# Kernel tuning notes

Hardware: AMD Instinct MI355X
Metric: run time of the kernel (lower is better)

Reference implementation:

```python
import jax, jax.numpy as jnp
import numpy as np

EMBED_DIM = 1024
NUM_HEADS = 16
HEAD_DIM = EMBED_DIM // NUM_HEADS


def setup_inputs() -> dict:
    key = jax.random.key(0)
    k1, k2, k3, k4, k5 = jax.random.split(key, 5)
    B, N, D = 2, 2048, EMBED_DIM
    s = 1.0 / np.sqrt(D)
    x = jax.random.normal(k1, (B, N, D), dtype=jnp.float32)
    qkv_w = jax.random.uniform(k2, (3 * D, D), minval=-s, maxval=s, dtype=jnp.float32)
    qkv_b = jax.random.uniform(k3, (3 * D,), minval=-s, maxval=s, dtype=jnp.float32)
    proj_w = jax.random.uniform(k4, (D, D), minval=-s, maxval=s, dtype=jnp.float32)
    proj_b = jax.random.uniform(k5, (D,), minval=-s, maxval=s, dtype=jnp.float32)
    return {"x": x, "qkv_w": qkv_w, "qkv_b": qkv_b, "proj_w": proj_w, "proj_b": proj_b}


def reference(x, qkv_w, qkv_b, proj_w, proj_b):
    B, N, D = x.shape
    H, Hd = NUM_HEADS, HEAD_DIM
    scale = Hd ** (-0.5)
    # QKV projection (torch Linear: x @ W.T + b)
    qkv = x @ qkv_w.T + qkv_b                      # [B, N, 3D]
    q, k, v = jnp.split(qkv, 3, axis=-1)
    def split_heads(t):
        return t.reshape(B, N, H, Hd).transpose(0, 2, 1, 3)  # [B, H, N, Hd]
    q, k, v = map(split_heads, (q, k, v))
    attn = jnp.einsum("bhqd,bhkd->bhqk", q, k) * scale       # [B, H, N, N]
    attn = jax.nn.softmax(attn, axis=-1)
    out = jnp.einsum("bhqk,bhkd->bhqd", attn, v)             # [B, H, N, Hd]
    out = out.transpose(0, 2, 1, 3).reshape(B, N, D)
    return out @ proj_w.T + proj_b
```

## Files before the change

kernel.cpp:

```cpp
#include <hip/hip_runtime.h>
#include <hip/hip_bf16.h>


#define DEV __device__ __forceinline__

typedef __attribute__((ext_vector_type(8))) __bf16 bf16x8;
typedef __attribute__((ext_vector_type(4))) float f32x4;

static DEV unsigned short f2bf(float f) {
  unsigned u = __builtin_bit_cast(unsigned, f);
  u += 0x7FFFu + ((u >> 16) & 1u);
  return (unsigned short)(u >> 16);
}

static DEV void gld16(const void* g, void* l) {
  __builtin_amdgcn_global_load_lds(
      (const __attribute__((address_space(1))) unsigned int*)g,
      (__attribute__((address_space(3))) unsigned int*)l, 16, 0, 0);
}

static DEV f32x4 mfma16(bf16x8 a, bf16x8 b, f32x4 c) {
  return __builtin_amdgcn_mfma_f32_16x16x32_bf16(a, b, c, 0, 0, 0);
}

__global__ void k_f2bf(const float* __restrict__ s, unsigned short* __restrict__ d) {
  int i = (blockIdx.x * 256 + threadIdx.x) * 4;
  float4 v = *reinterpret_cast<const float4*>(s + i);
  union { unsigned short h[4]; uint2 u; } cv;
  cv.h[0] = f2bf(v.x); cv.h[1] = f2bf(v.y); cv.h[2] = f2bf(v.z); cv.h[3] = f2bf(v.w);
  *reinterpret_cast<uint2*>(d + i) = cv.u;
}

__global__ __launch_bounds__(256) void k_qkv(
    const unsigned short* __restrict__ A, const unsigned short* __restrict__ W,
    const float* __restrict__ bias, unsigned short* __restrict__ Qb,
    unsigned short* __restrict__ Kb, unsigned short* __restrict__ Vt) {
  const int K = 1024;
  __shared__ __align__(16) unsigned short As[128 * 32], Bs[128 * 32];
  const int tid = threadIdx.x, lane = tid & 63, wid = tid >> 6;
  const int wm = wid >> 1, wn = wid & 1, fr = lane & 15, fg = lane >> 4;
  const size_t bm = blockIdx.x, bn = blockIdx.y;
  const unsigned short* gA = A + bm * 128 * K;
  const unsigned short* gW = W + bn * 128 * K;
  f32x4 acc[4][4] = {};
  for (int k0 = 0; k0 < K; k0 += 32) {
#pragma unroll
    for (int c = 0; c < 2; ++c) {
      int bi = c * 4096 + wid * 1024 + lane * 16;
      int row = bi >> 6, ce = (bi & 63) >> 1;
      gld16(gA + (size_t)row * K + k0 + ce, As + c * 2048 + wid * 512);
      gld16(gW + (size_t)row * K + k0 + ce, Bs + c * 2048 + wid * 512);
    }
    __syncthreads();
    bf16x8 af[4], bw[4];
#pragma unroll
    for (int m = 0; m < 4; ++m)
      af[m] = *reinterpret_cast<const bf16x8*>(As + (wm * 64 + m * 16 + fr) * 32 + fg * 8);
#pragma unroll
    for (int n = 0; n < 4; ++n)
      bw[n] = *reinterpret_cast<const bf16x8*>(Bs + (wn * 64 + n * 16 + fr) * 32 + fg * 8);
#pragma unroll
    for (int m = 0; m < 4; ++m)
#pragma unroll
      for (int n = 0; n < 4; ++n)
        acc[m][n] = mfma16(af[m], bw[n], acc[m][n]);
    __syncthreads();
  }
  float bv[4];
#pragma unroll
  for (int n = 0; n < 4; ++n) bv[n] = bias[bn * 128 + wn * 64 + n * 16 + fr];
#pragma unroll
  for (int m = 0; m < 4; ++m)
#pragma unroll
    for (int n = 0; n < 4; ++n)
#pragma unroll
      for (int r = 0; r < 4; ++r) {
        int row = wm * 64 + m * 16 + fg * 4 + r;
        int token = (int)bm * 128 + row;
        int b_ = token >> 11, nn = token & 2047;
        int f = (int)bn * 128 + wn * 64 + n * 16 + fr;
        float val = acc[m][n][r] + bv[n];
        int t = f >> 10, d = f & 1023, h = d >> 6, hd = d & 63;
        size_t bh = (size_t)(b_ * 16 + h);
        if (t == 0)      Qb[(bh * 2048 + nn) * 64 + hd] = f2bf(val * 0.125f);
        else if (t == 1) Kb[(bh * 2048 + nn) * 64 + hd] = f2bf(val);
        else             Vt[(bh * 64 + hd) * 2048 + nn] = f2bf(val);
      }
}

__global__ __launch_bounds__(256) void k_attn(
    const unsigned short* __restrict__ Qb, const unsigned short* __restrict__ Kb,
    const unsigned short* __restrict__ Vt, unsigned short* __restrict__ Ob) {
  __shared__ __align__(16) unsigned short Ks[2][64 * 64];
  __shared__ __align__(16) unsigned short Vs[2][64 * 64];
  __shared__ __align__(16) unsigned short p_lds[4][16 * 64];
  const int tid = threadIdx.x, lane = tid & 63, w = tid >> 6;
  const int fr = lane & 15, fg = lane >> 4;
  const int bid = (int)(blockIdx.x & 7) * 128 + (int)(blockIdx.x >> 3);
  const int qt = bid & 31, bh = bid >> 5;
  const unsigned short* Qp = Qb + ((size_t)bh * 2048 + qt * 64 + w * 16) * 64;
  const unsigned short* Kp = Kb + (size_t)bh * 2048 * 64;
  const unsigned short* Vp = Vt + (size_t)bh * 64 * 2048;

  const int crow0 = w * 16 + (lane >> 3);
  bf16x8 qf[2];
#pragma unroll
  for (int ks = 0; ks < 2; ++ks)
    qf[ks] = *reinterpret_cast<const bf16x8*>(Qp + fr * 64 + ks * 32 + fg * 8);

  f32x4 accO[4] = {};
  float mrow = -1e30f, lpart = 0.f;

#define STAGE(bufi, kti)                                                      \
  {                                                                           \
    const unsigned short* Kt_ = Kp + (kti) * 64 * 64;                         \
    _Pragma("unroll")                                                         \
    for (int j = 0; j < 2; ++j) {                                             \
      int cr = crow0 + j * 8;                                                 \
      int cs = (lane & 7) ^ (cr & 7);                                         \
      gld16(Kt_ + cr * 64 + cs * 8, &Ks[bufi][(w * 2 + j) * 512]);            \
      gld16(Vp + (size_t)cr * 2048 + (kti) * 64 + cs * 8,                     \
            &Vs[bufi][(w * 2 + j) * 512]);                                    \
    }                                                                         \
  }

  STAGE(0, 0);
  __syncthreads();
  int buf = 0;
  for (int kt = 0; kt < 32; ++kt) {
    if (kt < 31) STAGE(buf ^ 1, kt + 1);
    f32x4 s[4] = {};
#pragma unroll
    for (int nf = 0; nf < 4; ++nf)
#pragma unroll
      for (int ks = 0; ks < 2; ++ks) {
        bf16x8 kf = *reinterpret_cast<const bf16x8*>(
            &Ks[buf][(nf * 16 + fr) * 64 + (((ks * 4 + fg) ^ (fr & 7)) * 8)]);
        s[nf] = mfma16(kf, qf[ks], s[nf]);
      }
    bf16x8 vf[2][4];
#pragma unroll
    for (int ks = 0; ks < 2; ++ks)
#pragma unroll
      for (int df = 0; df < 4; ++df)
        vf[ks][df] = *reinterpret_cast<const bf16x8*>(
            &Vs[buf][(df * 16 + fr) * 64 + (((ks * 4 + fg) ^ (fr & 7)) * 8)]);
    float mymax = fmaxf(
        fmaxf(fmaxf(fmaxf(s[0][0], s[0][1]), fmaxf(s[0][2], s[0][3])),
              fmaxf(fmaxf(s[1][0], s[1][1]), fmaxf(s[1][2], s[1][3]))),
        fmaxf(fmaxf(fmaxf(s[2][0], s[2][1]), fmaxf(s[2][2], s[2][3])),
              fmaxf(fmaxf(s[3][0], s[3][1]), fmaxf(s[3][2], s[3][3]))));
    if (!__all(mymax <= mrow + 8.0f)) {
      float pmax = mymax;
      pmax = fmaxf(pmax, __shfl_xor(pmax, 16));
      pmax = fmaxf(pmax, __shfl_xor(pmax, 32));
      float mnew = fmaxf(mrow, pmax);
      float sc = __expf(mrow - mnew);
      mrow = mnew;
      lpart *= sc;
      float scq[4];
#pragma unroll
      for (int r = 0; r < 4; ++r) scq[r] = __shfl(sc, fg * 4 + r);
#pragma unroll
      for (int df = 0; df < 4; ++df)
#pragma unroll
        for (int r = 0; r < 4; ++r) accO[df][r] *= scq[r];
    }
    float rs = 0.f;
#pragma unroll
    for (int nf = 0; nf < 4; ++nf)
#pragma unroll
      for (int r = 0; r < 4; ++r) {
        float p = __expf(s[nf][r] - mrow);
        s[nf][r] = p;
        rs += p;
      }
    lpart += rs;
#pragma unroll
    for (int nf = 0; nf < 4; ++nf) {
      union { unsigned short h[4]; uint2 u; } pk;
#pragma unroll
      for (int r = 0; r < 4; ++r) pk.h[r] = f2bf(s[nf][r]);
      *reinterpret_cast<uint2*>(
          &p_lds[w][fr * 64 + (((2 * nf + (fg >> 1)) ^ (fr & 7)) * 8) +
                   (fg & 1) * 4]) = pk.u;
    }
    bf16x8 pf[2];
#pragma unroll
    for (int ks = 0; ks < 2; ++ks)
      pf[ks] = *reinterpret_cast<const bf16x8*>(
          &p_lds[w][fr * 64 + (((ks * 4 + fg) ^ (fr & 7)) * 8)]);
#pragma unroll
    for (int df = 0; df < 4; ++df)
#pragma unroll
      for (int ks = 0; ks < 2; ++ks)
        accO[df] = mfma16(pf[ks], vf[ks][df], accO[df]);
    __syncthreads();
    buf ^= 1;
  }
#undef STAGE
  float lrow = lpart;
  lrow += __shfl_xor(lrow, 16);
  lrow += __shfl_xor(lrow, 32);
  float linv = 1.f / lrow;
  float lq[4];
#pragma unroll
  for (int r = 0; r < 4; ++r) lq[r] = __shfl(linv, fg * 4 + r);
  const int b_ = bh >> 4, h = bh & 15;
#pragma unroll
  for (int df = 0; df < 4; ++df)
#pragma unroll
    for (int r = 0; r < 4; ++r) {
      int nn = qt * 64 + w * 16 + fg * 4 + r;
      int d = df * 16 + fr;
      Ob[(size_t)(b_ * 2048 + nn) * 1024 + h * 64 + d] = f2bf(accO[df][r] * lq[r]);
    }
}

__global__ __launch_bounds__(256) void k_proj(
    const unsigned short* __restrict__ A, const unsigned short* __restrict__ W,
    const float* __restrict__ bias, float* __restrict__ out) {
  const int K = 1024;
  __shared__ __align__(16) unsigned short As[128 * 32], Bs[128 * 32];
  const int tid = threadIdx.x, lane = tid & 63, wid = tid >> 6;
  const int wm = wid >> 1, wn = wid & 1, fr = lane & 15, fg = lane >> 4;
  const size_t bm = blockIdx.x, bn = blockIdx.y;
  const unsigned short* gA = A + bm * 128 * K;
  const unsigned short* gW = W + bn * 128 * K;
  f32x4 acc[4][4] = {};
  for (int k0 = 0; k0 < K; k0 += 32) {
#pragma unroll
    for (int c = 0; c < 2; ++c) {
      int bi = c * 4096 + wid * 1024 + lane * 16;
      int row = bi >> 6, ce = (bi & 63) >> 1;
      gld16(gA + (size_t)row * K + k0 + ce, As + c * 2048 + wid * 512);
      gld16(gW + (size_t)row * K + k0 + ce, Bs + c * 2048 + wid * 512);
    }
    __syncthreads();
    bf16x8 af[4], bw[4];
#pragma unroll
    for (int m = 0; m < 4; ++m)
      af[m] = *reinterpret_cast<const bf16x8*>(As + (wm * 64 + m * 16 + fr) * 32 + fg * 8);
#pragma unroll
    for (int n = 0; n < 4; ++n)
      bw[n] = *reinterpret_cast<const bf16x8*>(Bs + (wn * 64 + n * 16 + fr) * 32 + fg * 8);
#pragma unroll
    for (int m = 0; m < 4; ++m)
#pragma unroll
      for (int n = 0; n < 4; ++n)
        acc[m][n] = mfma16(af[m], bw[n], acc[m][n]);
    __syncthreads();
  }
  float bv[4];
#pragma unroll
  for (int n = 0; n < 4; ++n) bv[n] = bias[bn * 128 + wn * 64 + n * 16 + fr];
#pragma unroll
  for (int m = 0; m < 4; ++m)
#pragma unroll
    for (int n = 0; n < 4; ++n)
#pragma unroll
      for (int r = 0; r < 4; ++r) {
        size_t token = bm * 128 + wm * 64 + m * 16 + fg * 4 + r;
        int f = (int)bn * 128 + wn * 64 + n * 16 + fr;
        out[token * 1024 + f] = acc[m][n][r] + bv[n];
      }
}

extern "C" void kernel_launch(void* const* d_in, const int* in_sizes, int n_in,
                              void* d_out, int out_size, void* d_ws, size_t ws_size,
                              hipStream_t stream) {
  const float* x      = (const float*)d_in[0];
  const float* qkv_w  = (const float*)d_in[1];
  const float* qkv_b  = (const float*)d_in[2];
  const float* proj_w = (const float*)d_in[3];
  const float* proj_b = (const float*)d_in[4];
  float* out = (float*)d_out;
  char* ws = (char*)d_ws;
  unsigned short* xb  = (unsigned short*)(ws);
  unsigned short* wqb = (unsigned short*)(ws + (size_t)(8u << 20));
  unsigned short* pwb = (unsigned short*)(ws + (size_t)(14u << 20));
  unsigned short* Qb  = (unsigned short*)(ws + (size_t)(16u << 20));
  unsigned short* Kb  = (unsigned short*)(ws + (size_t)(24u << 20));
  unsigned short* Vt  = (unsigned short*)(ws + (size_t)(32u << 20));
  unsigned short* Ob  = (unsigned short*)(ws + (size_t)(40u << 20));

  k_f2bf<<<4096, 256, 0, stream>>>(x, xb);
  k_f2bf<<<3072, 256, 0, stream>>>(qkv_w, wqb);
  k_f2bf<<<1024, 256, 0, stream>>>(proj_w, pwb);
  k_qkv<<<dim3(32, 24), 256, 0, stream>>>(xb, wqb, qkv_b, Qb, Kb, Vt);
  k_attn<<<1024, 256, 0, stream>>>(Qb, Kb, Vt, Ob);
  k_proj<<<dim3(32, 8), 256, 0, stream>>>(Ob, pwb, proj_b, out);
}
```

Measured before the change: 224.0 us.

## Fuse conversion kernels, use exp2 softmax, restructure attention double-buffer loop

```diff
diff --git a/kernel.cpp b/kernel.cpp
--- a/kernel.cpp
+++ b/kernel.cpp
@@ -13,6 +13,18 @@
   return (unsigned short)(u >> 16);
 }
 
+static DEV float fexp2(float x) {
+#if __has_builtin(__builtin_amdgcn_exp2f)
+  return __builtin_amdgcn_exp2f(x);
+#else
+  return __expf(x * 0.69314718055994531f);
+#endif
+}
+
+static DEV float max3(float a, float b, float c) {
+  return fmaxf(fmaxf(a, b), c);
+}
+
 static DEV void gld16(const void* g, void* l) {
   __builtin_amdgcn_global_load_lds(
       (const __attribute__((address_space(1))) unsigned int*)g,
@@ -23,8 +35,17 @@
   return __builtin_amdgcn_mfma_f32_16x16x32_bf16(a, b, c, 0, 0, 0);
 }
 
-__global__ void k_f2bf(const float* __restrict__ s, unsigned short* __restrict__ d) {
-  int i = (blockIdx.x * 256 + threadIdx.x) * 4;
+__global__ void k_conv(const float* __restrict__ x, const float* __restrict__ qw,
+                       const float* __restrict__ pw, unsigned short* __restrict__ xb,
+                       unsigned short* __restrict__ wqb, unsigned short* __restrict__ pwb) {
+  int b = blockIdx.x;
+  const float* s;
+  unsigned short* d;
+  int base;
+  if (b < 4096)      { s = x;  d = xb;  base = b; }
+  else if (b < 7168) { s = qw; d = wqb; base = b - 4096; }
+  else               { s = pw; d = pwb; base = b - 7168; }
+  int i = (base * 256 + threadIdx.x) * 4;
   float4 v = *reinterpret_cast<const float4*>(s + i);
   union { unsigned short h[4]; uint2 u; } cv;
   cv.h[0] = f2bf(v.x); cv.h[1] = f2bf(v.y); cv.h[2] = f2bf(v.z); cv.h[3] = f2bf(v.w);
@@ -66,33 +87,109 @@
         acc[m][n] = mfma16(af[m], bw[n], acc[m][n]);
     __syncthreads();
   }
+  const float QSCALE = 0.18033688011112043f;
   float bv[4];
 #pragma unroll
   for (int n = 0; n < 4; ++n) bv[n] = bias[bn * 128 + wn * 64 + n * 16 + fr];
 #pragma unroll
   for (int m = 0; m < 4; ++m)
 #pragma unroll
-    for (int n = 0; n < 4; ++n)
-#pragma unroll
-      for (int r = 0; r < 4; ++r) {
-        int row = wm * 64 + m * 16 + fg * 4 + r;
-        int token = (int)bm * 128 + row;
-        int b_ = token >> 11, nn = token & 2047;
-        int f = (int)bn * 128 + wn * 64 + n * 16 + fr;
-        float val = acc[m][n][r] + bv[n];
-        int t = f >> 10, d = f & 1023, h = d >> 6, hd = d & 63;
-        size_t bh = (size_t)(b_ * 16 + h);
-        if (t == 0)      Qb[(bh * 2048 + nn) * 64 + hd] = f2bf(val * 0.125f);
-        else if (t == 1) Kb[(bh * 2048 + nn) * 64 + hd] = f2bf(val);
-        else             Vt[(bh * 64 + hd) * 2048 + nn] = f2bf(val);
+    for (int n = 0; n < 4; ++n) {
+      int f = (int)bn * 128 + wn * 64 + n * 16 + fr;
+      int t = f >> 10, d = f & 1023, h = d >> 6, hd = d & 63;
+      int token0 = (int)bm * 128 + wm * 64 + m * 16 + fg * 4;
+      int b_ = token0 >> 11, nn0 = token0 & 2047;
+      size_t bh = (size_t)(b_ * 16 + h);
+      float v0 = acc[m][n][0] + bv[n], v1 = acc[m][n][1] + bv[n];
+      float v2 = acc[m][n][2] + bv[n], v3 = acc[m][n][3] + bv[n];
+      if (t == 0) {
+        unsigned short* q = Qb + (bh * 2048 + nn0) * 64 + hd;
+        q[0] = f2bf(v0 * QSCALE); q[64] = f2bf(v1 * QSCALE);
+        q[128] = f2bf(v2 * QSCALE); q[192] = f2bf(v3 * QSCALE);
+      } else if (t == 1) {
+        unsigned short* k = Kb + (bh * 2048 + nn0) * 64 + hd;
+        k[0] = f2bf(v0); k[64] = f2bf(v1); k[128] = f2bf(v2); k[192] = f2bf(v3);
+      } else {
+        union { unsigned short h[4]; uint2 u; } pk;
+        pk.h[0] = f2bf(v0); pk.h[1] = f2bf(v1);
+        pk.h[2] = f2bf(v2); pk.h[3] = f2bf(v3);
+        *reinterpret_cast<uint2*>(Vt + (bh * 64 + hd) * 2048 + nn0) = pk.u;
       }
+    }
+}
+
+static DEV void attn_tile(const unsigned short* __restrict__ Ksb,
+                          const unsigned short* __restrict__ Vsb,
+                          unsigned short* __restrict__ pw, const bf16x8* qf,
+                          int fr, int fg, f32x4* accO, float& mrow, float& lpart) {
+  f32x4 s[4] = {};
+#pragma unroll
+  for (int nf = 0; nf < 4; ++nf)
+#pragma unroll
+    for (int ks = 0; ks < 2; ++ks) {
+      bf16x8 kf = *reinterpret_cast<const bf16x8*>(
+          &Ksb[(nf * 16 + fr) * 64 + (((ks * 4 + fg) ^ (fr & 7)) * 8)]);
+      s[nf] = mfma16(kf, qf[ks], s[nf]);
+    }
+  bf16x8 vf[2][4];
+#pragma unroll
+  for (int ks = 0; ks < 2; ++ks)
+#pragma unroll
+    for (int df = 0; df < 4; ++df)
+      vf[ks][df] = *reinterpret_cast<const bf16x8*>(
+          &Vsb[(df * 16 + fr) * 64 + (((ks * 4 + fg) ^ (fr & 7)) * 8)]);
+  float m0 = max3(s[0][0], s[0][1], s[0][2]);
+  float m1 = max3(s[0][3], s[1][0], s[1][1]);
+  float m2 = max3(s[1][2], s[1][3], s[2][0]);
+  float m3 = max3(s[2][1], s[2][2], s[2][3]);
+  float m4 = max3(s[3][0], s[3][1], s[3][2]);
+  float mymax = fmaxf(max3(m0, m1, m2), max3(m3, m4, s[3][3]));
+  if (!__all(mymax <= mrow + 8.0f)) {
+    float pmax = fmaxf(mymax, __shfl_xor(mymax, 16));
+    pmax = fmaxf(pmax, __shfl_xor(pmax, 32));
+    float mnew = fmaxf(mrow, pmax);
+    float sc = fexp2(mrow - mnew);
+    mrow = mnew;
+    lpart *= sc;
+    float scq[4];
+#pragma unroll
+    for (int r = 0; r < 4; ++r) scq[r] = __shfl(sc, fg * 4 + r);
+#pragma unroll
+    for (int df = 0; df < 4; ++df)
+#pragma unroll
+      for (int r = 0; r < 4; ++r) accO[df][r] *= scq[r];
+  }
+  float rs = 0.f;
+#pragma unroll
+  for (int nf = 0; nf < 4; ++nf) {
+    union { unsigned short h[4]; uint2 u; } pk;
+#pragma unroll
+    for (int r = 0; r < 4; ++r) {
+      float p = fexp2(s[nf][r] - mrow);
+      pk.h[r] = f2bf(p);
+      rs += p;
+    }
+    *reinterpret_cast<uint2*>(
+        &pw[fr * 64 + (((2 * nf + (fg >> 1)) ^ (fr & 7)) * 8) + (fg & 1) * 4]) = pk.u;
+  }
+  lpart += rs;
+  bf16x8 pf[2];
+#pragma unroll
+  for (int ks = 0; ks < 2; ++ks)
+    pf[ks] = *reinterpret_cast<const bf16x8*>(
+        &pw[fr * 64 + (((ks * 4 + fg) ^ (fr & 7)) * 8)]);
+#pragma unroll
+  for (int df = 0; df < 4; ++df)
+#pragma unroll
+    for (int ks = 0; ks < 2; ++ks)
+      accO[df] = mfma16(pf[ks], vf[ks][df], accO[df]);
 }
 
 __global__ __launch_bounds__(256) void k_attn(
     const unsigned short* __restrict__ Qb, const unsigned short* __restrict__ Kb,
     const unsigned short* __restrict__ Vt, unsigned short* __restrict__ Ob) {
-  __shared__ __align__(16) unsigned short Ks[2][64 * 64];
-  __shared__ __align__(16) unsigned short Vs[2][64 * 64];
+  __shared__ __align__(16) unsigned short Ks0[64 * 64], Ks1[64 * 64];
+  __shared__ __align__(16) unsigned short Vs0[64 * 64], Vs1[64 * 64];
   __shared__ __align__(16) unsigned short p_lds[4][16 * 64];
   const int tid = threadIdx.x, lane = tid & 63, w = tid >> 6;
   const int fr = lane & 15, fg = lane >> 4;
@@ -101,6 +198,7 @@
   const unsigned short* Qp = Qb + ((size_t)bh * 2048 + qt * 64 + w * 16) * 64;
   const unsigned short* Kp = Kb + (size_t)bh * 2048 * 64;
   const unsigned short* Vp = Vt + (size_t)bh * 64 * 2048;
+  unsigned short* pw = &p_lds[w][0];
 
   const int crow0 = w * 16 + (lane >> 3);
   bf16x8 qf[2];
@@ -111,92 +209,29 @@
   f32x4 accO[4] = {};
   float mrow = -1e30f, lpart = 0.f;
 
-#define STAGE(bufi, kti)                                                      \
+#define STAGE(KDST, VDST, kti)                                                \
   {                                                                           \
     const unsigned short* Kt_ = Kp + (kti) * 64 * 64;                         \
     _Pragma("unroll")                                                         \
     for (int j = 0; j < 2; ++j) {                                             \
       int cr = crow0 + j * 8;                                                 \
       int cs = (lane & 7) ^ (cr & 7);                                         \
-      gld16(Kt_ + cr * 64 + cs * 8, &Ks[bufi][(w * 2 + j) * 512]);            \
+      gld16(Kt_ + cr * 64 + cs * 8, (KDST) + (w * 2 + j) * 512);              \
       gld16(Vp + (size_t)cr * 2048 + (kti) * 64 + cs * 8,                     \
-            &Vs[bufi][(w * 2 + j) * 512]);                                    \
+            (VDST) + (w * 2 + j) * 512);                                      \
     }                                                                         \
   }
 
-  STAGE(0, 0);
+  STAGE(Ks0, Vs0, 0);
+  STAGE(Ks1, Vs1, 1);
   __syncthreads();
-  int buf = 0;
-  for (int kt = 0; kt < 32; ++kt) {
-    if (kt < 31) STAGE(buf ^ 1, kt + 1);
-    f32x4 s[4] = {};
-#pragma unroll
-    for (int nf = 0; nf < 4; ++nf)
-#pragma unroll
-      for (int ks = 0; ks < 2; ++ks) {
-        bf16x8 kf = *reinterpret_cast<const bf16x8*>(
-            &Ks[buf][(nf * 16 + fr) * 64 + (((ks * 4 + fg) ^ (fr & 7)) * 8)]);
-        s[nf] = mfma16(kf, qf[ks], s[nf]);
-      }
-    bf16x8 vf[2][4];
-#pragma unroll
-    for (int ks = 0; ks < 2; ++ks)
-#pragma unroll
-      for (int df = 0; df < 4; ++df)
-        vf[ks][df] = *reinterpret_cast<const bf16x8*>(
-            &Vs[buf][(df * 16 + fr) * 64 + (((ks * 4 + fg) ^ (fr & 7)) * 8)]);
-    float mymax = fmaxf(
-        fmaxf(fmaxf(fmaxf(s[0][0], s[0][1]), fmaxf(s[0][2], s[0][3])),
-              fmaxf(fmaxf(s[1][0], s[1][1]), fmaxf(s[1][2], s[1][3]))),
-        fmaxf(fmaxf(fmaxf(s[2][0], s[2][1]), fmaxf(s[2][2], s[2][3])),
-              fmaxf(fmaxf(s[3][0], s[3][1]), fmaxf(s[3][2], s[3][3]))));
-    if (!__all(mymax <= mrow + 8.0f)) {
-      float pmax = mymax;
-      pmax = fmaxf(pmax, __shfl_xor(pmax, 16));
-      pmax = fmaxf(pmax, __shfl_xor(pmax, 32));
-      float mnew = fmaxf(mrow, pmax);
-      float sc = __expf(mrow - mnew);
-      mrow = mnew;
-      lpart *= sc;
-      float scq[4];
-#pragma unroll
-      for (int r = 0; r < 4; ++r) scq[r] = __shfl(sc, fg * 4 + r);
-#pragma unroll
-      for (int df = 0; df < 4; ++df)
-#pragma unroll
-        for (int r = 0; r < 4; ++r) accO[df][r] *= scq[r];
-    }
-    float rs = 0.f;
-#pragma unroll
-    for (int nf = 0; nf < 4; ++nf)
-#pragma unroll
-      for (int r = 0; r < 4; ++r) {
-        float p = __expf(s[nf][r] - mrow);
-        s[nf][r] = p;
-        rs += p;
-      }
-    lpart += rs;
-#pragma unroll
-    for (int nf = 0; nf < 4; ++nf) {
-      union { unsigned short h[4]; uint2 u; } pk;
-#pragma unroll
-      for (int r = 0; r < 4; ++r) pk.h[r] = f2bf(s[nf][r]);
-      *reinterpret_cast<uint2*>(
-          &p_lds[w][fr * 64 + (((2 * nf + (fg >> 1)) ^ (fr & 7)) * 8) +
-                   (fg & 1) * 4]) = pk.u;
-    }
-    bf16x8 pf[2];
-#pragma unroll
-    for (int ks = 0; ks < 2; ++ks)
-      pf[ks] = *reinterpret_cast<const bf16x8*>(
-          &p_lds[w][fr * 64 + (((ks * 4 + fg) ^ (fr & 7)) * 8)]);
-#pragma unroll
-    for (int df = 0; df < 4; ++df)
-#pragma unroll
-      for (int ks = 0; ks < 2; ++ks)
-        accO[df] = mfma16(pf[ks], vf[ks][df], accO[df]);
-    __syncthreads();
-    buf ^= 1;
+  for (int i = 0; i < 16; ++i) {
+    attn_tile(Ks0, Vs0, pw, qf, fr, fg, accO, mrow, lpart);
+    __syncthreads();
+    if (i < 15) STAGE(Ks0, Vs0, 2 * i + 2);
+    attn_tile(Ks1, Vs1, pw, qf, fr, fg, accO, mrow, lpart);
+    __syncthreads();
+    if (i < 15) STAGE(Ks1, Vs1, 2 * i + 3);
   }
 #undef STAGE
   float lrow = lpart;
@@ -284,9 +319,7 @@
   unsigned short* Vt  = (unsigned short*)(ws + (size_t)(32u << 20));
   unsigned short* Ob  = (unsigned short*)(ws + (size_t)(40u << 20));
 
-  k_f2bf<<<4096, 256, 0, stream>>>(x, xb);
-  k_f2bf<<<3072, 256, 0, stream>>>(qkv_w, wqb);
-  k_f2bf<<<1024, 256, 0, stream>>>(proj_w, pwb);
+  k_conv<<<8192, 256, 0, stream>>>(x, qkv_w, proj_w, xb, wqb, pwb);
   k_qkv<<<dim3(32, 24), 256, 0, stream>>>(xb, wqb, qkv_b, Qb, Kb, Vt);
   k_attn<<<1024, 256, 0, stream>>>(Qb, Kb, Vt, Ob);
   k_proj<<<dim3(32, 8), 256, 0, stream>>>(Ob, pwb, proj_b, out);
```

New measurement: 206.2 us. 8.0% less time.
